# Optimization experiments

Measured on AMD Instinct MI355X. Metric: run time of the kernel, lower is better.

Reference implementation:

```python
import jax, jax.numpy as jnp
import numpy as np

EPS = 1e-5  # torch nn.LayerNorm default eps
N_SUBJECTS = 16


def _gelu(x):
    # torch nn.GELU default = exact erf formulation
    return jax.nn.gelu(x, approximate=False)


def setup_inputs() -> dict:
    key = jax.random.key(0)
    ks = jax.random.split(key, 8)
    B, D = 131072, 512
    x = jax.random.normal(ks[0], (B, D), dtype=jnp.float32)
    groups = jax.random.randint(ks[1], (B,), 0, N_SUBJECTS, dtype=jnp.int32)
    # LayerNorm affine params: rows 0..15 subject-specific, row 16 = default_norm
    gammas = jnp.ones((N_SUBJECTS + 1, D), dtype=jnp.float32)
    betas = jnp.zeros((N_SUBJECTS + 1, D), dtype=jnp.float32)
    # Domain classifier MLP (xavier-uniform weights, zero biases)
    def xavier(k, fan_in, fan_out):
        lim = np.sqrt(6.0 / (fan_in + fan_out)).astype(np.float32)
        return jax.random.uniform(k, (fan_in, fan_out), dtype=jnp.float32,
                                  minval=-lim, maxval=lim)
    W1 = xavier(ks[2], D, 256); b1 = jnp.zeros((256,), jnp.float32)
    W2 = xavier(ks[3], 256, 128); b2 = jnp.zeros((128,), jnp.float32)
    W3 = xavier(ks[4], 128, N_SUBJECTS); b3 = jnp.zeros((N_SUBJECTS,), jnp.float32)
    return {"x": x, "groups": groups, "gammas": gammas, "betas": betas,
            "W1": W1, "b1": b1, "W2": W2, "b2": b2, "W3": W3, "b3": b3}


def _subject_layernorm(x, groups, gammas, betas):
    # Fused per-row LayerNorm with per-subject affine params.
    # Out-of-range subject ids (>= N_SUBJECTS or < 0) use the default row (index N_SUBJECTS).
    valid = (groups >= 0) & (groups < N_SUBJECTS)
    idx = jnp.where(valid, groups, N_SUBJECTS)
    g = gammas[idx]  # (B, D)
    b = betas[idx]   # (B, D)
    mu = jnp.mean(x, axis=-1, keepdims=True)
    var = jnp.mean(jnp.square(x - mu), axis=-1, keepdims=True)  # biased, as torch LN
    xn = (x - mu) * jax.lax.rsqrt(var + EPS)
    return xn * g + b


def _domain_classifier(x, W1, b1, W2, b2, W3, b3):
    # Dropout is identity in eval mode
    h = _gelu(x @ W1 + b1)
    h = _gelu(h @ W2 + b2)
    return h @ W3 + b3


def reference(x, groups, gammas, betas, W1, b1, W2, b2, W3, b3):
    # gradient reversal is identity in forward
    domain_logits = _domain_classifier(x, W1, b1, W2, b2, W3, b3)
    normalized_x = _subject_layernorm(x, groups, gammas, betas)
    return (normalized_x, domain_logits)
```

## Files before the change

### kernel.cpp

```cpp
#include <hip/hip_runtime.h>
#include <hip/hip_bf16.h>
#include <stdint.h>

#define NSUB 16

typedef short  bf16x8 __attribute__((ext_vector_type(8)));
typedef float  f32x4  __attribute__((ext_vector_type(4)));
typedef unsigned int u32x4 __attribute__((ext_vector_type(4)));

__device__ __forceinline__ float gelu_exact(float x){
  return 0.5f * x * (1.0f + erff(x * 0.70710678118654752440f));
}

__device__ __forceinline__ float gelu_fast(float x){
  float xx = x * x;
  float m  = fmaf(0.044715f, xx, 1.0f);
  float a  = x * m * -2.3022084f;
  float e  = __builtin_amdgcn_exp2f(a);
  float r  = __builtin_amdgcn_rcpf(e + 1.0f);
  return x * r;
}

__device__ __forceinline__ unsigned short f2bf(float f){
  union { float f; uint32_t u; } v; v.f = f;
  uint32_t u = v.u;
  return (unsigned short)((u + 0x7FFFu + ((u >> 16) & 1u)) >> 16);
}

__device__ __forceinline__ unsigned int pk2(float lo, float hi){
  union { __hip_bfloat162 b; unsigned int u; } c;
  c.b = __float22bfloat162_rn(make_float2(lo, hi));
  return c.u;
}

__device__ __forceinline__ bf16x8 as_bf(u32x4 v){
  union { u32x4 u; bf16x8 b; } c; c.u = v; return c.b;
}

__device__ __forceinline__ float bflo(unsigned int u){
  union { unsigned int u; float f; } c; c.u = u << 16; return c.f;
}
__device__ __forceinline__ float bfhi(unsigned int u){
  union { unsigned int u; float f; } c; c.u = u & 0xffff0000u; return c.f;
}

__global__ __launch_bounds__(256) void wconv_kernel(
    const float* __restrict__ W1, const float* __restrict__ W2, const float* __restrict__ W3,
    unsigned short* __restrict__ W1f, unsigned short* __restrict__ W2f, unsigned short* __restrict__ W3f){
  int t = blockIdx.x * 256 + threadIdx.x;
  if (t < 131072){
    int n = t >> 9, k = t & 511;
    int lane = ((k >> 3) & 3) * 16 + (n & 15);
    int idx = (((k >> 5) * 16 + (n >> 4)) * 64 + lane) * 8 + (k & 7);
    W1f[idx] = f2bf(W1[k*256 + n]);
  } else if (t < 163840){
    int i = t - 131072; int n = i >> 8, k = i & 255;
    int lane = ((k >> 3) & 3) * 16 + (n & 15);
    int idx = (((k >> 5) * 8 + (n >> 4)) * 64 + lane) * 8 + (k & 7);
    W2f[idx] = f2bf(W2[k*128 + n]);
  } else if (t < 165888){
    int i = t - 163840; int n = i >> 7, k = i & 127;
    int lane = ((k >> 3) & 3) * 16 + n;
    int idx = ((k >> 5) * 64 + lane) * 8 + (k & 7);
    W3f[idx] = f2bf(W3[k*16 + n]);
  }
}

__global__ __launch_bounds__(512, 4) void fused_kernel(
    const float* __restrict__ x, const int* __restrict__ groups,
    const float* __restrict__ gammas, const float* __restrict__ betas,
    const unsigned short* __restrict__ W1f, const float* __restrict__ b1,
    const unsigned short* __restrict__ W2f, const float* __restrict__ b2,
    const unsigned short* __restrict__ W3f, const float* __restrict__ b3,
    float* __restrict__ ln_out, float* __restrict__ out2){
  __shared__ __align__(16) uint8_t smem[65536];
  constexpr int OFF_H2 = 32768;

  const int tid  = threadIdx.x;
  const int wave = tid >> 6;
  const int lane = tid & 63;
  const int l15  = lane & 15;
  const int g4   = lane >> 4;
  const int row0 = blockIdx.x * 64;

  const int sr  = tid >> 3;
  const int sc  = tid & 7;
  const int swz = (sr & 7) << 4;
  const int wb  = (sc*16) ^ swz;
  uint8_t* xrow = smem + sr*1024;
  const float* xg = x + (size_t)(row0 + sr)*512 + sc*8;

  int gi   = groups[row0 + sr];
  int gidx = ((unsigned)gi < (unsigned)NSUB) ? gi : NSUB;

  float s = 0.f, q = 0.f;
  #pragma unroll
  for (int t = 0; t < 8; ++t){
    f32x4 v0 = *(const f32x4*)(xg + t*64);
    f32x4 v1 = *(const f32x4*)(xg + t*64 + 4);
    s += v0.x + v0.y + v0.z + v0.w + v1.x + v1.y + v1.z + v1.w;
    q += v0.x*v0.x + v0.y*v0.y + v0.z*v0.z + v0.w*v0.w
       + v1.x*v1.x + v1.y*v1.y + v1.z*v1.z + v1.w*v1.w;
    u32x4 pw;
    pw.x = pk2(v0.x, v0.y); pw.y = pk2(v0.z, v0.w);
    pw.z = pk2(v1.x, v1.y); pw.w = pk2(v1.z, v1.w);
    *(u32x4*)(xrow + t*128 + wb) = pw;
  }
  s += __shfl_xor(s, 1); s += __shfl_xor(s, 2); s += __shfl_xor(s, 4);
  q += __shfl_xor(q, 1); q += __shfl_xor(q, 2); q += __shfl_xor(q, 4);
  float mu  = s * (1.0f/512.0f);
  float var = q * (1.0f/512.0f) - mu*mu;
  float rs  = rsqrtf(var + 1e-5f);
  float nmr = -mu * rs;

  u32x4 braw[4][2];
  #pragma unroll
  for (int p = 0; p < 3; ++p)
    #pragma unroll
    for (int n = 0; n < 2; ++n)
      braw[p][n] = *(const u32x4*)(W1f + (size_t)(((p*16 + wave*2 + n)*64 + lane)*8));

  float b1v[2];
  #pragma unroll
  for (int n = 0; n < 2; ++n) b1v[n] = b1[wave*32 + n*16 + l15];
  float b2v = b2[wave*16 + l15];
  float b3v = b3[l15];

  {
    const float* gpr = gammas + (size_t)gidx*512 + sc*8;
    const float* bpr = betas  + (size_t)gidx*512 + sc*8;
    float* op = ln_out + (size_t)(row0 + sr)*512 + sc*8;
    #pragma unroll
    for (int t = 0; t < 8; ++t){
      u32x4 pw = *(const u32x4*)(xrow + t*128 + wb);
      f32x4 g0 = *(const f32x4*)(gpr + t*64);
      f32x4 g1 = *(const f32x4*)(gpr + t*64 + 4);
      f32x4 e0 = *(const f32x4*)(bpr + t*64);
      f32x4 e1 = *(const f32x4*)(bpr + t*64 + 4);
      f32x4 o0, o1;
      o0.x = fmaf(fmaf(bflo(pw.x), rs, nmr), g0.x, e0.x);
      o0.y = fmaf(fmaf(bfhi(pw.x), rs, nmr), g0.y, e0.y);
      o0.z = fmaf(fmaf(bflo(pw.y), rs, nmr), g0.z, e0.z);
      o0.w = fmaf(fmaf(bfhi(pw.y), rs, nmr), g0.w, e0.w);
      o1.x = fmaf(fmaf(bflo(pw.z), rs, nmr), g1.x, e1.x);
      o1.y = fmaf(fmaf(bfhi(pw.z), rs, nmr), g1.y, e1.y);
      o1.z = fmaf(fmaf(bflo(pw.w), rs, nmr), g1.z, e1.z);
      o1.w = fmaf(fmaf(bfhi(pw.w), rs, nmr), g1.w, e1.w);
      *(f32x4*)(op + t*64)     = o0;
      *(f32x4*)(op + t*64 + 4) = o1;
    }
  }

  int baseA[4][2];
  #pragma unroll
  for (int m = 0; m < 4; ++m){
    int row = m*16 + l15;
    int sw  = (row & 7) << 4;
    int bse = row*1024 + ((g4*16) ^ (sw & 0x30));
    int kx  = (row >> 2) & 1;
    baseA[m][0] = bse + ((0 ^ kx) << 6);
    baseA[m][1] = bse + ((1 ^ kx) << 6);
  }

  __syncthreads();

  f32x4 acc1[4][2] = {};
  #pragma unroll
  for (int g = 0; g < 16; ++g){
    if (g < 13){
      #pragma unroll
      for (int n = 0; n < 2; ++n)
        braw[(g+3)&3][n] = *(const u32x4*)(W1f + (size_t)((((g+3)*16 + wave*2 + n)*64 + lane)*8));
    }
    bf16x8 a[4];
    #pragma unroll
    for (int m = 0; m < 4; ++m)
      a[m] = *(const bf16x8*)(smem + baseA[m][g & 1] + (g >> 1)*128);
    #pragma unroll
    for (int m = 0; m < 4; ++m)
      #pragma unroll
      for (int n = 0; n < 2; ++n)
        acc1[m][n] = __builtin_amdgcn_mfma_f32_16x16x32_bf16(a[m], as_bf(braw[g & 3][n]), acc1[m][n], 0, 0, 0);
  }

  u32x4 b2raw[4];
  #pragma unroll
  for (int p = 0; p < 3; ++p)
    b2raw[p] = *(const u32x4*)(W2f + (size_t)(((p*8 + wave)*64 + lane)*8));

  __syncthreads();

  #pragma unroll
  for (int n = 0; n < 2; ++n){
    #pragma unroll
    for (int m = 0; m < 4; ++m){
      #pragma unroll
      for (int r = 0; r < 4; ++r){
        int row = m*16 + g4*4 + r;
        int col = wave*32 + n*16 + l15;
        float v = gelu_fast(acc1[m][n][r] + b1v[n]);
        *(unsigned short*)(smem + row*512 + ((col*2) ^ ((row & 7) << 4))) = f2bf(v);
      }
    }
  }
  __syncthreads();

  int baseH[4][2];
  #pragma unroll
  for (int m = 0; m < 4; ++m){
    int row = m*16 + l15;
    int sw  = (row & 7) << 4;
    int bse = row*512 + ((g4*16) ^ (sw & 0x30));
    int kx  = (row >> 2) & 1;
    baseH[m][0] = bse + ((0 ^ kx) << 6);
    baseH[m][1] = bse + ((1 ^ kx) << 6);
  }
  f32x4 acc2[4] = {};
  #pragma unroll
  for (int g = 0; g < 8; ++g){
    if (g < 5)
      b2raw[(g+3)&3] = *(const u32x4*)(W2f + (size_t)((((g+3)*8 + wave)*64 + lane)*8));
    bf16x8 a[4];
    #pragma unroll
    for (int m = 0; m < 4; ++m)
      a[m] = *(const bf16x8*)(smem + baseH[m][g & 1] + (g >> 1)*128);
    #pragma unroll
    for (int m = 0; m < 4; ++m)
      acc2[m] = __builtin_amdgcn_mfma_f32_16x16x32_bf16(a[m], as_bf(b2raw[g & 3]), acc2[m], 0, 0, 0);
  }

  u32x4 b3raw[4];
  #pragma unroll
  for (int ks = 0; ks < 4; ++ks)
    b3raw[ks] = *(const u32x4*)(W3f + (size_t)((ks*64 + lane)*8));

  #pragma unroll
  for (int m = 0; m < 4; ++m){
    #pragma unroll
    for (int r = 0; r < 4; ++r){
      int row = m*16 + g4*4 + r;
      int col = wave*16 + l15;
      float v = gelu_fast(acc2[m][r] + b2v);
      *(unsigned short*)(smem + OFF_H2 + row*256 + ((col*2) ^ ((row & 7) << 4))) = f2bf(v);
    }
  }
  __syncthreads();

  if (wave < 4){
    int baseG[2];
    {
      int row = wave*16 + l15;
      int sw  = (row & 7) << 4;
      int bse = OFF_H2 + row*256 + ((g4*16) ^ (sw & 0x30));
      int kx  = (row >> 2) & 1;
      baseG[0] = bse + ((0 ^ kx) << 6);
      baseG[1] = bse + ((1 ^ kx) << 6);
    }
    f32x4 acc3 = {};
    #pragma unroll
    for (int ks = 0; ks < 4; ++ks){
      bf16x8 a = *(const bf16x8*)(smem + baseG[ks & 1] + (ks >> 1)*128);
      acc3 = __builtin_amdgcn_mfma_f32_16x16x32_bf16(a, as_bf(b3raw[ks]), acc3, 0, 0, 0);
    }
    #pragma unroll
    for (int r = 0; r < 4; ++r){
      int grow = row0 + wave*16 + g4*4 + r;
      out2[(size_t)grow*16 + l15] = acc3[r] + b3v;
    }
  }
}

__global__ __launch_bounds__(256) void ln_kernel(
    const float* __restrict__ x, const int* __restrict__ groups,
    const float* __restrict__ gammas, const float* __restrict__ betas,
    float* __restrict__ out){
  int row  = blockIdx.x * 4 + (threadIdx.x >> 6);
  int lane = threadIdx.x & 63;
  const float4* xr = (const float4*)(x + (size_t)row * 512);
  float4 a = xr[lane];
  float4 b = xr[lane + 64];
  float s = a.x + a.y + a.z + a.w + b.x + b.y + b.z + b.w;
  float q = a.x*a.x + a.y*a.y + a.z*a.z + a.w*a.w
          + b.x*b.x + b.y*b.y + b.z*b.z + b.w*b.w;
  #pragma unroll
  for (int o = 32; o > 0; o >>= 1){
    s += __shfl_xor(s, o);
    q += __shfl_xor(q, o);
  }
  float mu  = s * (1.0f/512.0f);
  float var = q * (1.0f/512.0f) - mu*mu;
  float rsq = rsqrtf(var + 1e-5f);
  int gi = groups[row];
  int idx = ((unsigned)gi < (unsigned)NSUB) ? gi : NSUB;
  const float4* gr = (const float4*)(gammas + (size_t)idx * 512);
  const float4* br = (const float4*)(betas  + (size_t)idx * 512);
  float4 g0 = gr[lane], g1 = gr[lane + 64];
  float4 e0 = br[lane], e1 = br[lane + 64];
  float4 o0, o1;
  o0.x = (a.x - mu)*rsq*g0.x + e0.x; o0.y = (a.y - mu)*rsq*g0.y + e0.y;
  o0.z = (a.z - mu)*rsq*g0.z + e0.z; o0.w = (a.w - mu)*rsq*g0.w + e0.w;
  o1.x = (b.x - mu)*rsq*g1.x + e1.x; o1.y = (b.y - mu)*rsq*g1.y + e1.y;
  o1.z = (b.z - mu)*rsq*g1.z + e1.z; o1.w = (b.w - mu)*rsq*g1.w + e1.w;
  float4* orow = (float4*)(out + (size_t)row * 512);
  orow[lane]      = o0;
  orow[lane + 64] = o1;
}

__global__ __launch_bounds__(256) void mlp_naive(
    const float* __restrict__ x,
    const float* __restrict__ W1, const float* __restrict__ b1,
    const float* __restrict__ W2, const float* __restrict__ b2,
    const float* __restrict__ W3, const float* __restrict__ b3,
    float* __restrict__ out2){
  __shared__ float xr[512];
  __shared__ float h1[256];
  __shared__ float h2[128];
  int row = blockIdx.x, t = threadIdx.x;
  xr[t]       = x[(size_t)row*512 + t];
  xr[t + 256] = x[(size_t)row*512 + t + 256];
  __syncthreads();
  {
    float s = 0.f;
    for (int k = 0; k < 512; ++k) s += xr[k] * W1[k*256 + t];
    h1[t] = gelu_exact(s + b1[t]);
  }
  __syncthreads();
  if (t < 128){
    float s = 0.f;
    for (int k = 0; k < 256; ++k) s += h1[k] * W2[k*128 + t];
    h2[t] = gelu_exact(s + b2[t]);
  }
  __syncthreads();
  if (t < 16){
    float s = 0.f;
    for (int k = 0; k < 128; ++k) s += h2[k] * W3[k*16 + t];
    out2[(size_t)row*16 + t] = s + b3[t];
  }
}

extern "C" void kernel_launch(void* const* d_in, const int* in_sizes, int n_in,
                              void* d_out, int out_size, void* d_ws, size_t ws_size,
                              hipStream_t stream){
  const float* x      = (const float*)d_in[0];
  const int*   groups = (const int*)d_in[1];
  const float* gammas = (const float*)d_in[2];
  const float* betas  = (const float*)d_in[3];
  const float* W1 = (const float*)d_in[4];
  const float* b1 = (const float*)d_in[5];
  const float* W2 = (const float*)d_in[6];
  const float* b2 = (const float*)d_in[7];
  const float* W3 = (const float*)d_in[8];
  const float* b3 = (const float*)d_in[9];
  float* out  = (float*)d_out;
  const int B = in_sizes[0] / 512;
  float* out2 = out + (size_t)B * 512;

  const int n_u16 = 131072 + 32768 + 2048;
  const size_t ws_need = (size_t)n_u16 * sizeof(unsigned short);
  if (ws_size >= ws_need){
    unsigned short* W1f = (unsigned short*)d_ws;
    unsigned short* W2f = W1f + 131072;
    unsigned short* W3f = W2f + 32768;
    wconv_kernel<<<(n_u16 + 255)/256, 256, 0, stream>>>(W1, W2, W3, W1f, W2f, W3f);
    fused_kernel<<<B/64, 512, 0, stream>>>(x, groups, gammas, betas,
                                           W1f, b1, W2f, b2, W3f, b3, out, out2);
  } else {
    mlp_naive<<<B, 256, 0, stream>>>(x, W1, b1, W2, b2, W3, b3, out2);
    ln_kernel<<<B/4, 256, 0, stream>>>(x, groups, gammas, betas, out);
  }
}
```

Measured before the change: 155.5 us.

## Specialize waves: four run the MLP GEMMs, four compute LayerNorm from fp32 x

Splits the 512-thread block into two roles. Waves 0-3 run the three MLP GEMMs with wider N tiles per wave. Waves 4-7 re-read x from global memory in fp32 and compute the LayerNorm output in two 32-row batches, overlapped with the GEMM phases. This hides the LayerNorm store traffic behind MFMA work and uses exact fp32 inputs instead of bf16-rounded smem values. The cost is reading x twice, higher register pressure in the GEMM waves from larger accumulators, and only half the waves issuing MFMAs.

```diff
diff --git a/kernel.cpp b/kernel.cpp
--- a/kernel.cpp
+++ b/kernel.cpp
@@ -35,13 +35,6 @@
 
 __device__ __forceinline__ bf16x8 as_bf(u32x4 v){
   union { u32x4 u; bf16x8 b; } c; c.u = v; return c.b;
-}
-
-__device__ __forceinline__ float bflo(unsigned int u){
-  union { unsigned int u; float f; } c; c.u = u << 16; return c.f;
-}
-__device__ __forceinline__ float bfhi(unsigned int u){
-  union { unsigned int u; float f; } c; c.u = u & 0xffff0000u; return c.f;
 }
 
 __global__ __launch_bounds__(256) void wconv_kernel(
@@ -66,6 +59,47 @@
   }
 }
 
+__device__ __forceinline__ void ln_do(const f32x4* xr, int grow, int lsc,
+    const int* __restrict__ groups, const float* __restrict__ gammas,
+    const float* __restrict__ betas, float* __restrict__ ln_out){
+  float s = 0.f, q = 0.f;
+  #pragma unroll
+  for (int i = 0; i < 16; ++i){
+    s += xr[i].x + xr[i].y + xr[i].z + xr[i].w;
+    q += xr[i].x*xr[i].x + xr[i].y*xr[i].y + xr[i].z*xr[i].z + xr[i].w*xr[i].w;
+  }
+  s += __shfl_xor(s, 1); s += __shfl_xor(s, 2); s += __shfl_xor(s, 4);
+  q += __shfl_xor(q, 1); q += __shfl_xor(q, 2); q += __shfl_xor(q, 4);
+  float mu  = s * (1.0f/512.0f);
+  float var = q * (1.0f/512.0f) - mu*mu;
+  float rs  = rsqrtf(var + 1e-5f);
+  float nmr = -mu * rs;
+  int gi   = groups[grow];
+  int gidx = ((unsigned)gi < (unsigned)NSUB) ? gi : NSUB;
+  const float* gpr = gammas + (size_t)gidx*512 + lsc*8;
+  const float* bpr = betas  + (size_t)gidx*512 + lsc*8;
+  float* op = ln_out + (size_t)grow*512 + lsc*8;
+  #pragma unroll
+  for (int t = 0; t < 8; ++t){
+    f32x4 g0 = *(const f32x4*)(gpr + t*64);
+    f32x4 g1 = *(const f32x4*)(gpr + t*64 + 4);
+    f32x4 e0 = *(const f32x4*)(bpr + t*64);
+    f32x4 e1 = *(const f32x4*)(bpr + t*64 + 4);
+    f32x4 a = xr[2*t], b = xr[2*t+1];
+    f32x4 o0, o1;
+    o0.x = fmaf(fmaf(a.x, rs, nmr), g0.x, e0.x);
+    o0.y = fmaf(fmaf(a.y, rs, nmr), g0.y, e0.y);
+    o0.z = fmaf(fmaf(a.z, rs, nmr), g0.z, e0.z);
+    o0.w = fmaf(fmaf(a.w, rs, nmr), g0.w, e0.w);
+    o1.x = fmaf(fmaf(b.x, rs, nmr), g1.x, e1.x);
+    o1.y = fmaf(fmaf(b.y, rs, nmr), g1.y, e1.y);
+    o1.z = fmaf(fmaf(b.z, rs, nmr), g1.z, e1.z);
+    o1.w = fmaf(fmaf(b.w, rs, nmr), g1.w, e1.w);
+    *(f32x4*)(op + t*64)     = o0;
+    *(f32x4*)(op + t*64 + 4) = o1;
+  }
+}
+
 __global__ __launch_bounds__(512, 4) void fused_kernel(
     const float* __restrict__ x, const int* __restrict__ groups,
     const float* __restrict__ gammas, const float* __restrict__ betas,
@@ -82,171 +116,180 @@
   const int l15  = lane & 15;
   const int g4   = lane >> 4;
   const int row0 = blockIdx.x * 64;
-
-  const int sr  = tid >> 3;
-  const int sc  = tid & 7;
-  const int swz = (sr & 7) << 4;
-  const int wb  = (sc*16) ^ swz;
-  uint8_t* xrow = smem + sr*1024;
-  const float* xg = x + (size_t)(row0 + sr)*512 + sc*8;
-
-  int gi   = groups[row0 + sr];
-  int gidx = ((unsigned)gi < (unsigned)NSUB) ? gi : NSUB;
-
-  float s = 0.f, q = 0.f;
-  #pragma unroll
-  for (int t = 0; t < 8; ++t){
-    f32x4 v0 = *(const f32x4*)(xg + t*64);
-    f32x4 v1 = *(const f32x4*)(xg + t*64 + 4);
-    s += v0.x + v0.y + v0.z + v0.w + v1.x + v1.y + v1.z + v1.w;
-    q += v0.x*v0.x + v0.y*v0.y + v0.z*v0.z + v0.w*v0.w
-       + v1.x*v1.x + v1.y*v1.y + v1.z*v1.z + v1.w*v1.w;
-    u32x4 pw;
-    pw.x = pk2(v0.x, v0.y); pw.y = pk2(v0.z, v0.w);
-    pw.z = pk2(v1.x, v1.y); pw.w = pk2(v1.z, v1.w);
-    *(u32x4*)(xrow + t*128 + wb) = pw;
-  }
-  s += __shfl_xor(s, 1); s += __shfl_xor(s, 2); s += __shfl_xor(s, 4);
-  q += __shfl_xor(q, 1); q += __shfl_xor(q, 2); q += __shfl_xor(q, 4);
-  float mu  = s * (1.0f/512.0f);
-  float var = q * (1.0f/512.0f) - mu*mu;
-  float rs  = rsqrtf(var + 1e-5f);
-  float nmr = -mu * rs;
-
-  u32x4 braw[4][2];
-  #pragma unroll
-  for (int p = 0; p < 3; ++p)
-    #pragma unroll
-    for (int n = 0; n < 2; ++n)
-      braw[p][n] = *(const u32x4*)(W1f + (size_t)(((p*16 + wave*2 + n)*64 + lane)*8));
-
-  float b1v[2];
-  #pragma unroll
-  for (int n = 0; n < 2; ++n) b1v[n] = b1[wave*32 + n*16 + l15];
-  float b2v = b2[wave*16 + l15];
-  float b3v = b3[l15];
+  const bool is_gemm = (wave < 4);
 
   {
-    const float* gpr = gammas + (size_t)gidx*512 + sc*8;
-    const float* bpr = betas  + (size_t)gidx*512 + sc*8;
-    float* op = ln_out + (size_t)(row0 + sr)*512 + sc*8;
+    const int sr  = tid >> 3;
+    const int sc  = tid & 7;
+    const int wb  = (sc*16) ^ ((sr & 7) << 4);
+    uint8_t* xrow = smem + sr*1024;
+    const float* xg = x + (size_t)(row0 + sr)*512 + sc*8;
     #pragma unroll
     for (int t = 0; t < 8; ++t){
-      u32x4 pw = *(const u32x4*)(xrow + t*128 + wb);
-      f32x4 g0 = *(const f32x4*)(gpr + t*64);
-      f32x4 g1 = *(const f32x4*)(gpr + t*64 + 4);
-      f32x4 e0 = *(const f32x4*)(bpr + t*64);
-      f32x4 e1 = *(const f32x4*)(bpr + t*64 + 4);
-      f32x4 o0, o1;
-      o0.x = fmaf(fmaf(bflo(pw.x), rs, nmr), g0.x, e0.x);
-      o0.y = fmaf(fmaf(bfhi(pw.x), rs, nmr), g0.y, e0.y);
-      o0.z = fmaf(fmaf(bflo(pw.y), rs, nmr), g0.z, e0.z);
-      o0.w = fmaf(fmaf(bfhi(pw.y), rs, nmr), g0.w, e0.w);
-      o1.x = fmaf(fmaf(bflo(pw.z), rs, nmr), g1.x, e1.x);
-      o1.y = fmaf(fmaf(bfhi(pw.z), rs, nmr), g1.y, e1.y);
-      o1.z = fmaf(fmaf(bflo(pw.w), rs, nmr), g1.z, e1.z);
-      o1.w = fmaf(fmaf(bfhi(pw.w), rs, nmr), g1.w, e1.w);
-      *(f32x4*)(op + t*64)     = o0;
-      *(f32x4*)(op + t*64 + 4) = o1;
-    }
-  }
-
+      f32x4 v0 = *(const f32x4*)(xg + t*64);
+      f32x4 v1 = *(const f32x4*)(xg + t*64 + 4);
+      u32x4 pw;
+      pw.x = pk2(v0.x, v0.y); pw.y = pk2(v0.z, v0.w);
+      pw.z = pk2(v1.x, v1.y); pw.w = pk2(v1.z, v1.w);
+      *(u32x4*)(xrow + t*128 + wb) = pw;
+    }
+  }
+
+  u32x4 braw[2][4];
+  float b1v[4], b2v[2], b3v = 0.f;
   int baseA[4][2];
-  #pragma unroll
-  for (int m = 0; m < 4; ++m){
-    int row = m*16 + l15;
-    int sw  = (row & 7) << 4;
-    int bse = row*1024 + ((g4*16) ^ (sw & 0x30));
-    int kx  = (row >> 2) & 1;
-    baseA[m][0] = bse + ((0 ^ kx) << 6);
-    baseA[m][1] = bse + ((1 ^ kx) << 6);
-  }
-
-  __syncthreads();
-
-  f32x4 acc1[4][2] = {};
-  #pragma unroll
-  for (int g = 0; g < 16; ++g){
-    if (g < 13){
+  if (is_gemm){
+    #pragma unroll
+    for (int n = 0; n < 4; ++n)
+      braw[0][n] = *(const u32x4*)(W1f + (size_t)(((wave*4 + n)*64 + lane)*8));
+    #pragma unroll
+    for (int n = 0; n < 4; ++n) b1v[n] = b1[wave*64 + n*16 + l15];
+    #pragma unroll
+    for (int n = 0; n < 2; ++n) b2v[n] = b2[wave*32 + n*16 + l15];
+    b3v = b3[l15];
+    #pragma unroll
+    for (int m = 0; m < 4; ++m){
+      int row = m*16 + l15;
+      int sw  = (row & 7) << 4;
+      int bse = row*1024 + ((g4*16) ^ (sw & 0x30));
+      int kx  = (row >> 2) & 1;
+      baseA[m][0] = bse + ((0 ^ kx) << 6);
+      baseA[m][1] = bse + ((1 ^ kx) << 6);
+    }
+  }
+
+  f32x4 xr[16];
+  const int ltid = tid - 256;
+  const int lsc  = tid & 7;
+  if (!is_gemm){
+    const float* xa = x + (size_t)(row0 + (ltid >> 3))*512 + lsc*8;
+    #pragma unroll
+    for (int t = 0; t < 8; ++t){
+      xr[2*t]   = *(const f32x4*)(xa + t*64);
+      xr[2*t+1] = *(const f32x4*)(xa + t*64 + 4);
+    }
+  }
+
+  __syncthreads();
+
+  f32x4 acc1[4][4];
+  if (is_gemm){
+    #pragma unroll
+    for (int m = 0; m < 4; ++m)
+      #pragma unroll
+      for (int n = 0; n < 4; ++n)
+        acc1[m][n] = (f32x4){0.f, 0.f, 0.f, 0.f};
+    #pragma unroll
+    for (int g = 0; g < 16; ++g){
+      if (g < 15){
+        #pragma unroll
+        for (int n = 0; n < 4; ++n)
+          braw[(g+1)&1][n] = *(const u32x4*)(W1f + (size_t)((((g+1)*16 + wave*4 + n)*64 + lane)*8));
+      }
+      bf16x8 a[4];
+      #pragma unroll
+      for (int m = 0; m < 4; ++m)
+        a[m] = *(const bf16x8*)(smem + baseA[m][g & 1] + (g >> 1)*128);
+      #pragma unroll
+      for (int m = 0; m < 4; ++m)
+        #pragma unroll
+        for (int n = 0; n < 4; ++n)
+          acc1[m][n] = __builtin_amdgcn_mfma_f32_16x16x32_bf16(a[m], as_bf(braw[g & 1][n]), acc1[m][n], 0, 0, 0);
+    }
+  } else {
+    ln_do(xr, row0 + (ltid >> 3), lsc, groups, gammas, betas, ln_out);
+    const float* xb = x + (size_t)(row0 + 32 + (ltid >> 3))*512 + lsc*8;
+    #pragma unroll
+    for (int t = 0; t < 8; ++t){
+      xr[2*t]   = *(const f32x4*)(xb + t*64);
+      xr[2*t+1] = *(const f32x4*)(xb + t*64 + 4);
+    }
+  }
+
+  __syncthreads();
+
+  u32x4 b2raw[4][2];
+  if (is_gemm){
+    #pragma unroll
+    for (int p = 0; p < 3; ++p)
       #pragma unroll
       for (int n = 0; n < 2; ++n)
-        braw[(g+3)&3][n] = *(const u32x4*)(W1f + (size_t)((((g+3)*16 + wave*2 + n)*64 + lane)*8));
-    }
-    bf16x8 a[4];
+        b2raw[p][n] = *(const u32x4*)(W2f + (size_t)(((p*8 + wave*2 + n)*64 + lane)*8));
+    #pragma unroll
+    for (int n = 0; n < 4; ++n){
+      #pragma unroll
+      for (int m = 0; m < 4; ++m){
+        #pragma unroll
+        for (int r = 0; r < 4; ++r){
+          int row = m*16 + g4*4 + r;
+          int col = wave*64 + n*16 + l15;
+          float v = gelu_fast(acc1[m][n][r] + b1v[n]);
+          *(unsigned short*)(smem + row*512 + ((col*2) ^ ((row & 7) << 4))) = f2bf(v);
+        }
+      }
+    }
+  } else {
+    ln_do(xr, row0 + 32 + (ltid >> 3), lsc, groups, gammas, betas, ln_out);
+  }
+
+  __syncthreads();
+
+  u32x4 b3raw[4];
+  if (is_gemm){
+    int baseH[4][2];
+    #pragma unroll
+    for (int m = 0; m < 4; ++m){
+      int row = m*16 + l15;
+      int sw  = (row & 7) << 4;
+      int bse = row*512 + ((g4*16) ^ (sw & 0x30));
+      int kx  = (row >> 2) & 1;
+      baseH[m][0] = bse + ((0 ^ kx) << 6);
+      baseH[m][1] = bse + ((1 ^ kx) << 6);
+    }
+    f32x4 acc2[4][2];
     #pragma unroll
     for (int m = 0; m < 4; ++m)
-      a[m] = *(const bf16x8*)(smem + baseA[m][g & 1] + (g >> 1)*128);
-    #pragma unroll
-    for (int m = 0; m < 4; ++m)
       #pragma unroll
       for (int n = 0; n < 2; ++n)
-        acc1[m][n] = __builtin_amdgcn_mfma_f32_16x16x32_bf16(a[m], as_bf(braw[g & 3][n]), acc1[m][n], 0, 0, 0);
-  }
-
-  u32x4 b2raw[4];
-  #pragma unroll
-  for (int p = 0; p < 3; ++p)
-    b2raw[p] = *(const u32x4*)(W2f + (size_t)(((p*8 + wave)*64 + lane)*8));
-
-  __syncthreads();
-
-  #pragma unroll
-  for (int n = 0; n < 2; ++n){
-    #pragma unroll
-    for (int m = 0; m < 4; ++m){
-      #pragma unroll
-      for (int r = 0; r < 4; ++r){
-        int row = m*16 + g4*4 + r;
-        int col = wave*32 + n*16 + l15;
-        float v = gelu_fast(acc1[m][n][r] + b1v[n]);
-        *(unsigned short*)(smem + row*512 + ((col*2) ^ ((row & 7) << 4))) = f2bf(v);
+        acc2[m][n] = (f32x4){0.f, 0.f, 0.f, 0.f};
+    #pragma unroll
+    for (int g = 0; g < 8; ++g){
+      if (g < 5){
+        #pragma unroll
+        for (int n = 0; n < 2; ++n)
+          b2raw[(g+3)&3][n] = *(const u32x4*)(W2f + (size_t)((((g+3)*8 + wave*2 + n)*64 + lane)*8));
       }
-    }
-  }
-  __syncthreads();
-
-  int baseH[4][2];
-  #pragma unroll
-  for (int m = 0; m < 4; ++m){
-    int row = m*16 + l15;
-    int sw  = (row & 7) << 4;
-    int bse = row*512 + ((g4*16) ^ (sw & 0x30));
-    int kx  = (row >> 2) & 1;
-    baseH[m][0] = bse + ((0 ^ kx) << 6);
-    baseH[m][1] = bse + ((1 ^ kx) << 6);
-  }
-  f32x4 acc2[4] = {};
-  #pragma unroll
-  for (int g = 0; g < 8; ++g){
-    if (g < 5)
-      b2raw[(g+3)&3] = *(const u32x4*)(W2f + (size_t)((((g+3)*8 + wave)*64 + lane)*8));
-    bf16x8 a[4];
-    #pragma unroll
-    for (int m = 0; m < 4; ++m)
-      a[m] = *(const bf16x8*)(smem + baseH[m][g & 1] + (g >> 1)*128);
-    #pragma unroll
-    for (int m = 0; m < 4; ++m)
-      acc2[m] = __builtin_amdgcn_mfma_f32_16x16x32_bf16(a[m], as_bf(b2raw[g & 3]), acc2[m], 0, 0, 0);
-  }
-
-  u32x4 b3raw[4];
-  #pragma unroll
-  for (int ks = 0; ks < 4; ++ks)
-    b3raw[ks] = *(const u32x4*)(W3f + (size_t)((ks*64 + lane)*8));
-
-  #pragma unroll
-  for (int m = 0; m < 4; ++m){
-    #pragma unroll
-    for (int r = 0; r < 4; ++r){
-      int row = m*16 + g4*4 + r;
-      int col = wave*16 + l15;
-      float v = gelu_fast(acc2[m][r] + b2v);
-      *(unsigned short*)(smem + OFF_H2 + row*256 + ((col*2) ^ ((row & 7) << 4))) = f2bf(v);
-    }
-  }
-  __syncthreads();
-
-  if (wave < 4){
+      bf16x8 a[4];
+      #pragma unroll
+      for (int m = 0; m < 4; ++m)
+        a[m] = *(const bf16x8*)(smem + baseH[m][g & 1] + (g >> 1)*128);
+      #pragma unroll
+      for (int m = 0; m < 4; ++m)
+        #pragma unroll
+        for (int n = 0; n < 2; ++n)
+          acc2[m][n] = __builtin_amdgcn_mfma_f32_16x16x32_bf16(a[m], as_bf(b2raw[g & 3][n]), acc2[m][n], 0, 0, 0);
+    }
+    #pragma unroll
+    for (int ks = 0; ks < 4; ++ks)
+      b3raw[ks] = *(const u32x4*)(W3f + (size_t)((ks*64 + lane)*8));
+    #pragma unroll
+    for (int n = 0; n < 2; ++n){
+      #pragma unroll
+      for (int m = 0; m < 4; ++m){
+        #pragma unroll
+        for (int r = 0; r < 4; ++r){
+          int row = m*16 + g4*4 + r;
+          int col = wave*32 + n*16 + l15;
+          float v = gelu_fast(acc2[m][n][r] + b2v[n]);
+          *(unsigned short*)(smem + OFF_H2 + row*256 + ((col*2) ^ ((row & 7) << 4))) = f2bf(v);
+        }
+      }
+    }
+  }
+
+  __syncthreads();
+
+  if (is_gemm){
     int baseG[2];
     {
       int row = wave*16 + l15;
@@ -276,9 +319,9 @@
     float* __restrict__ out){
   int row  = blockIdx.x * 4 + (threadIdx.x >> 6);
   int lane = threadIdx.x & 63;
-  const float4* xr = (const float4*)(x + (size_t)row * 512);
-  float4 a = xr[lane];
-  float4 b = xr[lane + 64];
+  const float4* xrp = (const float4*)(x + (size_t)row * 512);
+  float4 a = xrp[lane];
+  float4 b = xrp[lane + 64];
   float s = a.x + a.y + a.z + a.w + b.x + b.y + b.z + b.w;
   float q = a.x*a.x + a.y*a.y + a.z*a.z + a.w*a.w
           + b.x*b.x + b.y*b.y + b.z*b.z + b.w*b.w;
```

Result: slower. 296.7 us (+90.8%).

## Split LayerNorm into separate specialized blocks alongside MLP blocks per stripe

Applied to the files above, without the earlier changes.

Launches three blocks per 64-row stripe: one runs the MLP on bf16-staged x, and two compute LayerNorm on 32 rows each directly from fp32 global loads. This removes the LN statistics and output writes from the MLP block's critical path and lets LN work overlap with MFMA work on other CUs. In exchange x is read twice from memory (relying on cache reuse between co-scheduled blocks), and LN now uses full-precision x instead of bf16-rounded values.

```diff
diff --git a/kernel.cpp b/kernel.cpp
--- a/kernel.cpp
+++ b/kernel.cpp
@@ -35,13 +35,6 @@
 
 __device__ __forceinline__ bf16x8 as_bf(u32x4 v){
   union { u32x4 u; bf16x8 b; } c; c.u = v; return c.b;
-}
-
-__device__ __forceinline__ float bflo(unsigned int u){
-  union { unsigned int u; float f; } c; c.u = u << 16; return c.f;
-}
-__device__ __forceinline__ float bfhi(unsigned int u){
-  union { unsigned int u; float f; } c; c.u = u & 0xffff0000u; return c.f;
 }
 
 __global__ __launch_bounds__(256) void wconv_kernel(
@@ -77,41 +70,84 @@
   constexpr int OFF_H2 = 32768;
 
   const int tid  = threadIdx.x;
+  const int stripe = blockIdx.x / 3;
+  const int role   = blockIdx.x - 3*stripe;
+  const int row0   = stripe * 64;
+
+  if (role != 0){
+    const int lrow0 = row0 + (role - 1) * 32;
+    const int sr = tid >> 4;
+    const int sc = tid & 15;
+    const float* xg = x + (size_t)(lrow0 + sr)*512 + sc*8;
+    f32x4 xr0[4], xr1[4];
+    #pragma unroll
+    for (int c = 0; c < 4; ++c){
+      xr0[c] = *(const f32x4*)(xg + c*128);
+      xr1[c] = *(const f32x4*)(xg + c*128 + 4);
+    }
+    float s = 0.f, q = 0.f;
+    #pragma unroll
+    for (int c = 0; c < 4; ++c){
+      s += xr0[c].x + xr0[c].y + xr0[c].z + xr0[c].w
+         + xr1[c].x + xr1[c].y + xr1[c].z + xr1[c].w;
+      q += xr0[c].x*xr0[c].x + xr0[c].y*xr0[c].y + xr0[c].z*xr0[c].z + xr0[c].w*xr0[c].w
+         + xr1[c].x*xr1[c].x + xr1[c].y*xr1[c].y + xr1[c].z*xr1[c].z + xr1[c].w*xr1[c].w;
+    }
+    s += __shfl_xor(s, 1); s += __shfl_xor(s, 2);
+    s += __shfl_xor(s, 4); s += __shfl_xor(s, 8);
+    q += __shfl_xor(q, 1); q += __shfl_xor(q, 2);
+    q += __shfl_xor(q, 4); q += __shfl_xor(q, 8);
+    float mu  = s * (1.0f/512.0f);
+    float var = q * (1.0f/512.0f) - mu*mu;
+    float rs  = rsqrtf(var + 1e-5f);
+    float nmr = -mu * rs;
+    int gi   = groups[lrow0 + sr];
+    int gidx = ((unsigned)gi < (unsigned)NSUB) ? gi : NSUB;
+    const float* gpr = gammas + (size_t)gidx*512 + sc*8;
+    const float* bpr = betas  + (size_t)gidx*512 + sc*8;
+    float* op = ln_out + (size_t)(lrow0 + sr)*512 + sc*8;
+    #pragma unroll
+    for (int c = 0; c < 4; ++c){
+      f32x4 g0 = *(const f32x4*)(gpr + c*128);
+      f32x4 g1 = *(const f32x4*)(gpr + c*128 + 4);
+      f32x4 e0 = *(const f32x4*)(bpr + c*128);
+      f32x4 e1 = *(const f32x4*)(bpr + c*128 + 4);
+      f32x4 o0, o1;
+      o0.x = fmaf(fmaf(xr0[c].x, rs, nmr), g0.x, e0.x);
+      o0.y = fmaf(fmaf(xr0[c].y, rs, nmr), g0.y, e0.y);
+      o0.z = fmaf(fmaf(xr0[c].z, rs, nmr), g0.z, e0.z);
+      o0.w = fmaf(fmaf(xr0[c].w, rs, nmr), g0.w, e0.w);
+      o1.x = fmaf(fmaf(xr1[c].x, rs, nmr), g1.x, e1.x);
+      o1.y = fmaf(fmaf(xr1[c].y, rs, nmr), g1.y, e1.y);
+      o1.z = fmaf(fmaf(xr1[c].z, rs, nmr), g1.z, e1.z);
+      o1.w = fmaf(fmaf(xr1[c].w, rs, nmr), g1.w, e1.w);
+      *(f32x4*)(op + c*128)     = o0;
+      *(f32x4*)(op + c*128 + 4) = o1;
+    }
+    return;
+  }
+
   const int wave = tid >> 6;
   const int lane = tid & 63;
   const int l15  = lane & 15;
   const int g4   = lane >> 4;
-  const int row0 = blockIdx.x * 64;
-
-  const int sr  = tid >> 3;
-  const int sc  = tid & 7;
-  const int swz = (sr & 7) << 4;
-  const int wb  = (sc*16) ^ swz;
-  uint8_t* xrow = smem + sr*1024;
-  const float* xg = x + (size_t)(row0 + sr)*512 + sc*8;
-
-  int gi   = groups[row0 + sr];
-  int gidx = ((unsigned)gi < (unsigned)NSUB) ? gi : NSUB;
-
-  float s = 0.f, q = 0.f;
-  #pragma unroll
-  for (int t = 0; t < 8; ++t){
-    f32x4 v0 = *(const f32x4*)(xg + t*64);
-    f32x4 v1 = *(const f32x4*)(xg + t*64 + 4);
-    s += v0.x + v0.y + v0.z + v0.w + v1.x + v1.y + v1.z + v1.w;
-    q += v0.x*v0.x + v0.y*v0.y + v0.z*v0.z + v0.w*v0.w
-       + v1.x*v1.x + v1.y*v1.y + v1.z*v1.z + v1.w*v1.w;
-    u32x4 pw;
-    pw.x = pk2(v0.x, v0.y); pw.y = pk2(v0.z, v0.w);
-    pw.z = pk2(v1.x, v1.y); pw.w = pk2(v1.z, v1.w);
-    *(u32x4*)(xrow + t*128 + wb) = pw;
-  }
-  s += __shfl_xor(s, 1); s += __shfl_xor(s, 2); s += __shfl_xor(s, 4);
-  q += __shfl_xor(q, 1); q += __shfl_xor(q, 2); q += __shfl_xor(q, 4);
-  float mu  = s * (1.0f/512.0f);
-  float var = q * (1.0f/512.0f) - mu*mu;
-  float rs  = rsqrtf(var + 1e-5f);
-  float nmr = -mu * rs;
+
+  {
+    const int sr  = tid >> 3;
+    const int sc  = tid & 7;
+    const int wb  = (sc*16) ^ ((sr & 7) << 4);
+    uint8_t* xrow = smem + sr*1024;
+    const float* xg = x + (size_t)(row0 + sr)*512 + sc*8;
+    #pragma unroll
+    for (int t = 0; t < 8; ++t){
+      f32x4 v0 = *(const f32x4*)(xg + t*64);
+      f32x4 v1 = *(const f32x4*)(xg + t*64 + 4);
+      u32x4 pw;
+      pw.x = pk2(v0.x, v0.y); pw.y = pk2(v0.z, v0.w);
+      pw.z = pk2(v1.x, v1.y); pw.w = pk2(v1.z, v1.w);
+      *(u32x4*)(xrow + t*128 + wb) = pw;
+    }
+  }
 
   u32x4 braw[4][2];
   #pragma unroll
@@ -125,31 +161,6 @@
   for (int n = 0; n < 2; ++n) b1v[n] = b1[wave*32 + n*16 + l15];
   float b2v = b2[wave*16 + l15];
   float b3v = b3[l15];
-
-  {
-    const float* gpr = gammas + (size_t)gidx*512 + sc*8;
-    const float* bpr = betas  + (size_t)gidx*512 + sc*8;
-    float* op = ln_out + (size_t)(row0 + sr)*512 + sc*8;
-    #pragma unroll
-    for (int t = 0; t < 8; ++t){
-      u32x4 pw = *(const u32x4*)(xrow + t*128 + wb);
-      f32x4 g0 = *(const f32x4*)(gpr + t*64);
-      f32x4 g1 = *(const f32x4*)(gpr + t*64 + 4);
-      f32x4 e0 = *(const f32x4*)(bpr + t*64);
-      f32x4 e1 = *(const f32x4*)(bpr + t*64 + 4);
-      f32x4 o0, o1;
-      o0.x = fmaf(fmaf(bflo(pw.x), rs, nmr), g0.x, e0.x);
-      o0.y = fmaf(fmaf(bfhi(pw.x), rs, nmr), g0.y, e0.y);
-      o0.z = fmaf(fmaf(bflo(pw.y), rs, nmr), g0.z, e0.z);
-      o0.w = fmaf(fmaf(bfhi(pw.y), rs, nmr), g0.w, e0.w);
-      o1.x = fmaf(fmaf(bflo(pw.z), rs, nmr), g1.x, e1.x);
-      o1.y = fmaf(fmaf(bfhi(pw.z), rs, nmr), g1.y, e1.y);
-      o1.z = fmaf(fmaf(bflo(pw.w), rs, nmr), g1.z, e1.z);
-      o1.w = fmaf(fmaf(bfhi(pw.w), rs, nmr), g1.w, e1.w);
-      *(f32x4*)(op + t*64)     = o0;
-      *(f32x4*)(op + t*64 + 4) = o1;
-    }
-  }
 
   int baseA[4][2];
   #pragma unroll
@@ -276,9 +287,9 @@
     float* __restrict__ out){
   int row  = blockIdx.x * 4 + (threadIdx.x >> 6);
   int lane = threadIdx.x & 63;
-  const float4* xr = (const float4*)(x + (size_t)row * 512);
-  float4 a = xr[lane];
-  float4 b = xr[lane + 64];
+  const float4* xrp = (const float4*)(x + (size_t)row * 512);
+  float4 a = xrp[lane];
+  float4 b = xrp[lane + 64];
   float s = a.x + a.y + a.z + a.w + b.x + b.y + b.z + b.w;
   float q = a.x*a.x + a.y*a.y + a.z*a.z + a.w*a.w
           + b.x*b.x + b.y*b.y + b.z*b.z + b.w*b.w;
@@ -362,8 +373,8 @@
     unsigned short* W2f = W1f + 131072;
     unsigned short* W3f = W2f + 32768;
     wconv_kernel<<<(n_u16 + 255)/256, 256, 0, stream>>>(W1, W2, W3, W1f, W2f, W3f);
-    fused_kernel<<<B/64, 512, 0, stream>>>(x, groups, gammas, betas,
-                                           W1f, b1, W2f, b2, W3f, b3, out, out2);
+    fused_kernel<<<3*(B/64), 512, 0, stream>>>(x, groups, gammas, betas,
+                                               W1f, b1, W2f, b2, W3f, b3, out, out2);
   } else {
     mlp_naive<<<B, 256, 0, stream>>>(x, W1, b1, W2, b2, W3, b3, out2);
     ln_kernel<<<B/4, 256, 0, stream>>>(x, groups, gammas, betas, out);
```

New measurement: 156.8 us. Within noise of the previous version (+0.8%).
